# Kernel tuning notes

Measured on AMD Instinct MI355X. Metric: run time of the kernel, lower is better.

## Reference

```python
import jax, jax.numpy as jnp
import numpy as np

B, M, D = 8, 1024, 1024
H = 16
HD = D // H  # 64
F = 4096

def layer_norm(x, gamma, beta, eps=1e-5):
    mu = jnp.mean(x, axis=-1, keepdims=True)
    var = jnp.var(x, axis=-1, keepdims=True)
    return (x - mu) * jax.lax.rsqrt(var + eps) * gamma + beta

def setup_inputs() -> dict:
    key = jax.random.key(0)
    ks = jax.random.split(key, 16)
    s = 0.02
    return {
        "h": jax.random.normal(ks[0], (B, M, D), jnp.float32),
        "h_all": jax.random.normal(ks[1], (B, M, D), jnp.float32),
        "Wq": jax.random.normal(ks[2], (D, D), jnp.float32) * s,
        "Wk": jax.random.normal(ks[3], (D, D), jnp.float32) * s,
        "Wv": jax.random.normal(ks[4], (D, D), jnp.float32) * s,
        "Wo": jax.random.normal(ks[5], (D, D), jnp.float32) * s,
        "W1": jax.random.normal(ks[6], (D, F), jnp.float32) * s,
        "b1": jnp.zeros((F,), jnp.float32),
        "W2": jax.random.normal(ks[7], (F, D), jnp.float32) * s,
        "b2": jnp.zeros((D,), jnp.float32),
        "g1": jnp.ones((D,), jnp.float32),
        "be1": jnp.zeros((D,), jnp.float32),
        "g2": jnp.ones((D,), jnp.float32),
        "be2": jnp.zeros((D,), jnp.float32),
    }

def reference(h, h_all, Wq, Wk, Wv, Wo, W1, b1, W2, b2, g1, be1, g2, be2):
    Bx, Mx, Dx = h.shape
    # projections (no bias, per nn.Linear(bias=False))
    q = (h @ Wq).reshape(Bx, Mx, H, HD)        # [B,M,H,hd]
    k = (h_all @ Wk).reshape(Bx, -1, H, HD)    # [B,N,H,hd]
    v = (h_all @ Wv).reshape(Bx, -1, H, HD)
    # attention: scale by sqrt(head_dim) as in SeqAttention(hidden_size=head_dim)
    scores = jnp.einsum('bqhd,bkhd->bhqk', q, k) / jnp.sqrt(jnp.float32(HD))
    attn = jax.nn.softmax(scores, axis=-1)
    ctx = jnp.einsum('bhqk,bkhd->bqhd', attn, v).reshape(Bx, Mx, Dx)
    attn_out = ctx @ Wo
    # post-norm residual 1
    h1 = layer_norm(h + attn_out, g1, be1)
    # FFN
    ff = jax.nn.relu(h1 @ W1 + b1) @ W2 + b2
    # post-norm residual 2
    out = layer_norm(h1 + ff, g2, be2)
    return out
```

## Files before the change

kernel.cpp:

```cpp
#include <hip/hip_runtime.h>
#include <hip/hip_bf16.h>

#define ROWS 8192
#define DD   1024
#define HH   16
#define HD   64
#define FF   4096

typedef __attribute__((ext_vector_type(4))) float f32x4;
typedef __attribute__((ext_vector_type(8))) __bf16 bf16x8;

static __device__ __forceinline__ unsigned short f2bf(float f) {
  unsigned u = __float_as_uint(f);
  u += 0x7fffu + ((u >> 16) & 1u);
  return (unsigned short)(u >> 16);
}

static __device__ __forceinline__ unsigned cvtpk_bf16(float lo, float hi) {
  unsigned r;
  asm("v_cvt_pk_bf16_f32 %0, %1, %2" : "=v"(r) : "v"(lo), "v"(hi));
  return r;
}

static __device__ __forceinline__ f32x4 mfma16(bf16x8 a, bf16x8 b, f32x4 c) {
  return __builtin_amdgcn_mfma_f32_16x16x32_bf16(a, b, c, 0, 0, 0);
}

#define GLOAD16(gp, lp) __builtin_amdgcn_global_load_lds( \
    (__attribute__((address_space(1))) void*)(gp), \
    (__attribute__((address_space(3))) void*)(lp), 16, 0, 0)

__global__ __launch_bounds__(256) void cast_bf16_k(
    const float* __restrict__ in, unsigned short* __restrict__ out, int n4) {
  int i = blockIdx.x * 256 + threadIdx.x;
  if (i >= n4) return;
  float4 v = ((const float4*)in)[i];
  ushort4 o;
  o.x = f2bf(v.x); o.y = f2bf(v.y); o.z = f2bf(v.z); o.w = f2bf(v.w);
  ((ushort4*)out)[i] = o;
}

__global__ __launch_bounds__(256) void transpose_cast_k(
    const float* __restrict__ in, unsigned short* __restrict__ out, int R, int C) {
  __shared__ float tile[32][33];
  int bx = blockIdx.x * 32;
  int by = blockIdx.y * 32;
  int tx = threadIdx.x, ty = threadIdx.y;
  #pragma unroll
  for (int i = 0; i < 32; i += 8)
    tile[ty + i][tx] = in[(size_t)(by + ty + i) * C + bx + tx];
  __syncthreads();
  #pragma unroll
  for (int i = 0; i < 32; i += 8)
    out[(size_t)(bx + ty + i) * R + by + tx] = f2bf(tile[tx][ty + i]);
}

template <int BM, int MODE, int KS = 1>
__global__ __launch_bounds__(512, 2) void gemm256(
    const unsigned short* __restrict__ A, const unsigned short* __restrict__ BT,
    const float* __restrict__ bias, void* __restrict__ Cout, void* __restrict__ Cout2,
    int Ni, int Ki, int nbx) {
  constexpr int MR = BM / 32;

  const int tid  = threadIdx.x;
  const int lane = tid & 63;
  const int wid  = tid >> 6;
  const int wm   = wid >> 2;
  const int wn   = wid & 3;
  const int lr   = lane & 15;
  const int kq   = lane >> 4;

  const int nwg = gridDim.x;
  const int cpx = nwg >> 3;
  const int wg  = (int)blockIdx.x;
  const int swz = (wg & 7) * cpx + (wg >> 3);
  const int perk = nwg / KS;
  const int kh   = swz / perk;
  const int swzr = swz % perk;
  const int bx = swzr % nbx, by = swzr / nbx;
  const int brow = by * BM, bcol = bx * 256;
  const int Kc   = Ki / KS;
  const int kbase = kh * Kc;

  f32x4 acc[MR][4] = {};
  const int NT = Kc >> 6;

  if constexpr (BM == 256) {
    __shared__ unsigned short As[2 * 2 * 256 * 32];
    __shared__ unsigned short Bs[2 * 2 * 256 * 32];

    const int srow0 = tid >> 2;
    const int csw   = ((tid & 3) ^ ((tid >> 3) & 3)) * 8;
    const size_t sA0 = (size_t)(brow + srow0) * Ki + kbase + csw;
    const size_t sB0 = (size_t)(bcol + srow0) * Ki + kbase + csw;
    const int coff = ((kq ^ ((lr >> 1) & 3)) << 4);

    auto stageu = [&](int srcT, int db, int ks) {
      const size_t so = (size_t)srcT * 64 + ks * 32;
      char* la = (char*)As + (db * 2 + ks) * 16384 + wid * 1024;
      char* lb = (char*)Bs + (db * 2 + ks) * 16384 + wid * 1024;
      GLOAD16(A + sA0 + so, la);
      GLOAD16(A + sA0 + so + (size_t)128 * Ki, la + 8192);
      GLOAD16(BT + sB0 + so, lb);
      GLOAD16(BT + sB0 + so + (size_t)128 * Ki, lb + 8192);
    };

    stageu(0, 0, 0);
    stageu(0, 0, 1);
    stageu(1, 1, 0);

    #pragma unroll 1
    for (int t = 0; t < NT; ++t) {
      const int d = t & 1;
      #pragma unroll
      for (int p = 0; p < 2; ++p) {
        asm volatile("s_waitcnt vmcnt(8)" ::: "memory");
        __builtin_amdgcn_s_barrier();
        __builtin_amdgcn_sched_barrier(0);
        const char* ab = (const char*)As + (d * 2 + p) * 16384;
        const char* bb = (const char*)Bs + (d * 2 + p) * 16384;
        bf16x8 af[8], bfv[4];
        #pragma unroll
        for (int m = 0; m < 8; ++m)
          af[m] = *(const bf16x8*)(ab + (wm * 128 + m * 16 + lr) * 64 + coff);
        #pragma unroll
        for (int n = 0; n < 4; ++n)
          bfv[n] = *(const bf16x8*)(bb + (wn * 64 + n * 16 + lr) * 64 + coff);
        if (p == 0) {
          const int ts = (t + 1 < NT) ? t + 1 : NT - 1;
          stageu(ts, (t + 1) & 1, 1);
        } else {
          const int ts = (t + 2 < NT) ? t + 2 : NT - 1;
          stageu(ts, d, 0);
        }
        __builtin_amdgcn_s_setprio(1);
        #pragma unroll
        for (int m = 0; m < 8; ++m)
          #pragma unroll
          for (int n = 0; n < 4; ++n)
            acc[m][n] = mfma16(af[m], bfv[n], acc[m][n]);
        __builtin_amdgcn_s_setprio(0);
      }
    }
    asm volatile("s_waitcnt vmcnt(0)" ::: "memory");
  } else {
    __shared__ unsigned short As[2][BM * 64];
    __shared__ unsigned short Bs[2][256 * 64];
    const int axor = (lr & 7) << 4;
    const int srow = wid * 8 + (lane >> 3);
    const int scol = ((lane & 7) * 8) ^ ((srow & 7) << 3);
    size_t offA[BM / 64], offB[4];
    #pragma unroll
    for (int L = 0; L < BM / 64; ++L)
      offA[L] = (size_t)(brow + L * 64 + srow) * Ki + kbase + scol;
    #pragma unroll
    for (int L = 0; L < 4; ++L)
      offB[L] = (size_t)(bcol + L * 64 + srow) * Ki + kbase + scol;

    auto stage = [&](int t, int d) {
      #pragma unroll
      for (int L = 0; L < BM / 64; ++L)
        GLOAD16(A + offA[L] + t * 64, (char*)As[d] + L * 8192 + wid * 1024);
      #pragma unroll
      for (int L = 0; L < 4; ++L)
        GLOAD16(BT + offB[L] + t * 64, (char*)Bs[d] + L * 8192 + wid * 1024);
    };

    stage(0, 0);
    stage(1, 1);

    #pragma unroll 1
    for (int t = 0; t < NT; ++t) {
      const int d = t & 1;
      asm volatile("s_waitcnt vmcnt(6)" ::: "memory");
      __builtin_amdgcn_s_barrier();
      __builtin_amdgcn_sched_barrier(0);

      const unsigned short* as = As[d];
      const unsigned short* bs = Bs[d];
      #pragma unroll
      for (int kk = 0; kk < 2; ++kk) {
        bf16x8 af[MR], bfv[4];
        #pragma unroll
        for (int m = 0; m < MR; ++m)
          af[m] = *(const bf16x8*)((const char*)as +
              (wm * (BM / 2) + m * 16 + lr) * 128 + ((kk * 64 + kq * 16) ^ axor));
        #pragma unroll
        for (int n = 0; n < 4; ++n)
          bfv[n] = *(const bf16x8*)((const char*)bs +
              (wn * 64 + n * 16 + lr) * 128 + ((kk * 64 + kq * 16) ^ axor));
        #pragma unroll
        for (int m = 0; m < MR; ++m)
          #pragma unroll
          for (int n = 0; n < 4; ++n)
            acc[m][n] = mfma16(af[m], bfv[n], acc[m][n]);
      }

      asm volatile("s_waitcnt lgkmcnt(0)" ::: "memory");
      __builtin_amdgcn_s_barrier();
      __builtin_amdgcn_sched_barrier(0);
      const int ts = (t + 2 < NT) ? t + 2 : NT - 1;
      stage(ts, d);
    }
  }

  #pragma unroll
  for (int m = 0; m < MR; ++m) {
    #pragma unroll
    for (int n = 0; n < 4; ++n) {
      const int r0 = brow + wm * (BM / 2) + m * 16 + kq * 4;
      const int c  = bcol + wn * 64 + n * 16 + lr;
      if constexpr (MODE == 4) {
        if (c < 1024) {
          #pragma unroll
          for (int e = 0; e < 4; ++e)
            ((unsigned short*)Cout)[(size_t)(r0 + e) * 1024 + c] = f2bf(acc[m][n][e]);
        } else {
          const int cc = c - 1024;
          const int bq = r0 >> 10;
          const int tok = r0 & 1023;
          ushort4 pk;
          pk.x = f2bf(acc[m][n][0]); pk.y = f2bf(acc[m][n][1]);
          pk.z = f2bf(acc[m][n][2]); pk.w = f2bf(acc[m][n][3]);
          *(ushort4*)((unsigned short*)Cout2 + ((size_t)bq * 1024 + cc) * 1024 + tok) = pk;
        }
      } else if constexpr (MODE == 5) {
        float* o = (kh == 0) ? (float*)Cout : (float*)Cout2;
        const float bv = (kh == 0) ? bias[c] : 0.0f;
        #pragma unroll
        for (int e = 0; e < 4; ++e)
          o[(size_t)(r0 + e) * Ni + c] = acc[m][n][e] + bv;
      } else {
        const float bv = (MODE == 2 || MODE == 3) ? bias[c] : 0.0f;
        #pragma unroll
        for (int e = 0; e < 4; ++e) {
          float v = acc[m][n][e] + bv;
          if (MODE == 2) v = fmaxf(v, 0.0f);
          if (MODE == 0 || MODE == 2)
            ((unsigned short*)Cout)[(size_t)(r0 + e) * Ni + c] = f2bf(v);
          else
            ((float*)Cout)[(size_t)(r0 + e) * Ni + c] = v;
        }
      }
    }
  }
}

__global__ __launch_bounds__(512, 6) void attn_k(
    const unsigned short* __restrict__ q, const unsigned short* __restrict__ k,
    const unsigned short* __restrict__ vT, unsigned short* __restrict__ ctx) {
  __shared__ unsigned short Ks[2][64 * 64];
  __shared__ unsigned short Vt[2][64 * 64];
  __shared__ unsigned short Ps[8][16 * 64];
  const int tid = threadIdx.x;
  const int lane = tid & 63;
  const int wid = tid >> 6;
  const int bh = blockIdx.x;
  const int b = bh >> 4, h = bh & 15;
  const int qrow0 = blockIdx.y * 128 + wid * 16;
  const size_t tokbase = (size_t)b * 1024;
  const int lr = lane & 15, kq = lane >> 4;

  const int srow = tid >> 3;
  const int scol = ((tid & 7) * 8) ^ ((srow & 7) << 3);
  const unsigned short* kg = k + (tokbase + srow) * 1024 + h * 64 + scol;
  const unsigned short* vg = vT + ((size_t)(b * 16 + h) * 64 + srow) * 1024 + scol;
  const int ldst = tid * 16;

  auto stage = [&](int kt, int d) {
    GLOAD16(kg + (size_t)kt * 64 * 1024, (char*)Ks[d] + ldst);
    GLOAD16(vg + kt * 64, (char*)Vt[d] + ldst);
  };

  bf16x8 aq[2];
  {
    const unsigned short* qp = q + (tokbase + qrow0 + lr) * DD + h * 64 + kq * 8;
    aq[0] = *(const bf16x8*)qp;
    aq[1] = *(const bf16x8*)(qp + 32);
  }

  float l_acc = 0.f;
  f32x4 acc[4] = {};
  const float C = 0.125f * 1.4426950408889634f;
  const unsigned swp = (unsigned)((lr & 7) << 4);
  const unsigned pbase = (unsigned)(lr * 128);

  stage(0, 0);
  stage(1, 1);

  #pragma unroll 2
  for (int kt = 0; kt < 16; ++kt) {
    const int d = kt & 1;
    asm volatile("s_waitcnt vmcnt(2)" ::: "memory");
    __builtin_amdgcn_s_barrier();
    __builtin_amdgcn_sched_barrier(0);

    f32x4 sv[4] = {};
    #pragma unroll
    for (int jb = 0; jb < 4; ++jb)
      #pragma unroll
      for (int ks = 0; ks < 2; ++ks) {
        int row = jb * 16 + lr;
        bf16x8 ak = *(const bf16x8*)((const char*)Ks[d] +
            row * 128 + ((ks * 64 + kq * 16) ^ ((row & 7) << 4)));
        sv[jb] = mfma16(ak, aq[ks], sv[jb]);
      }

    #pragma unroll
    for (int jb = 0; jb < 4; ++jb) {
      float p0 = exp2f(sv[jb][0] * C);
      float p1 = exp2f(sv[jb][1] * C);
      float p2 = exp2f(sv[jb][2] * C);
      float p3 = exp2f(sv[jb][3] * C);
      l_acc += (p0 + p1) + (p2 + p3);
      uint2 w;
      w.x = cvtpk_bf16(p0, p1);
      w.y = cvtpk_bf16(p2, p3);
      unsigned off = pbase + (((unsigned)(jb * 32 + kq * 8)) ^ swp);
      *(uint2*)((char*)Ps[wid] + off) = w;
    }

    #pragma unroll
    for (int ks = 0; ks < 2; ++ks) {
      bf16x8 ap = *(const bf16x8*)((const char*)Ps[wid] +
          lr * 128 + ((ks * 64 + kq * 16) ^ ((lr & 7) << 4)));
      #pragma unroll
      for (int db = 0; db < 4; ++db) {
        int dd = db * 16 + lr;
        bf16x8 bv = *(const bf16x8*)((const char*)Vt[d] +
            dd * 128 + ((ks * 64 + kq * 16) ^ ((dd & 7) << 4)));
        acc[db] = mfma16(bv, ap, acc[db]);
      }
    }

    asm volatile("s_waitcnt lgkmcnt(0)" ::: "memory");
    __builtin_amdgcn_s_barrier();
    __builtin_amdgcn_sched_barrier(0);
    const int ts = (kt + 2 < 16) ? kt + 2 : 15;
    stage(ts, d);
  }

  float l = l_acc + __shfl_xor(l_acc, 16);
  l += __shfl_xor(l, 32);
  const float inv = 1.0f / l;
  unsigned short* cp = ctx + (tokbase + qrow0 + lr) * DD + h * 64 + kq * 4;
  #pragma unroll
  for (int db = 0; db < 4; ++db) {
    ushort4 o;
    o.x = f2bf(acc[db][0] * inv);
    o.y = f2bf(acc[db][1] * inv);
    o.z = f2bf(acc[db][2] * inv);
    o.w = f2bf(acc[db][3] * inv);
    *(ushort4*)(cp + db * 16) = o;
  }
}

template <int WB>
__global__ __launch_bounds__(256) void ln_add_k(
    const float* __restrict__ a, const float* __restrict__ b,
    const float* __restrict__ gamma, const float* __restrict__ beta,
    float* __restrict__ outf, unsigned short* __restrict__ outb) {
  int row = blockIdx.x;
  int tid = threadIdx.x;
  size_t base = (size_t)row * 1024 + tid * 4;
  float4 va = *(const float4*)(a + base);
  float4 vb = *(const float4*)(b + base);
  float x[4] = {va.x + vb.x, va.y + vb.y, va.z + vb.z, va.w + vb.w};
  float s = x[0] + x[1] + x[2] + x[3];
  float sq = x[0] * x[0] + x[1] * x[1] + x[2] * x[2] + x[3] * x[3];
  #pragma unroll
  for (int mk = 1; mk < 64; mk <<= 1) {
    s += __shfl_xor(s, mk);
    sq += __shfl_xor(sq, mk);
  }
  __shared__ float red[8];
  int wid = tid >> 6, lane = tid & 63;
  if (lane == 0) { red[wid] = s; red[4 + wid] = sq; }
  __syncthreads();
  s = red[0] + red[1] + red[2] + red[3];
  sq = red[4] + red[5] + red[6] + red[7];
  float mu = s * (1.0f / 1024.0f);
  float var = sq * (1.0f / 1024.0f) - mu * mu;
  float rs = rsqrtf(var + 1e-5f);
  float4 g = *(const float4*)(gamma + tid * 4);
  float4 be = *(const float4*)(beta + tid * 4);
  float y[4];
  y[0] = (x[0] - mu) * rs * g.x + be.x;
  y[1] = (x[1] - mu) * rs * g.y + be.y;
  y[2] = (x[2] - mu) * rs * g.z + be.z;
  y[3] = (x[3] - mu) * rs * g.w + be.w;
  float4 o; o.x = y[0]; o.y = y[1]; o.z = y[2]; o.w = y[3];
  *(float4*)(outf + base) = o;
  if (WB) {
    ushort4 ob;
    ob.x = f2bf(y[0]); ob.y = f2bf(y[1]); ob.z = f2bf(y[2]); ob.w = f2bf(y[3]);
    *(ushort4*)(outb + base) = ob;
  }
}

__global__ __launch_bounds__(256) void ln3_k(
    const float* __restrict__ a, const float* __restrict__ b,
    const float* __restrict__ c,
    const float* __restrict__ gamma, const float* __restrict__ beta,
    float* __restrict__ outf) {
  int row = blockIdx.x;
  int tid = threadIdx.x;
  size_t base = (size_t)row * 1024 + tid * 4;
  float4 va = *(const float4*)(a + base);
  float4 vb = *(const float4*)(b + base);
  float4 vc = *(const float4*)(c + base);
  float x[4] = {va.x + vb.x + vc.x, va.y + vb.y + vc.y,
                va.z + vb.z + vc.z, va.w + vb.w + vc.w};
  float s = x[0] + x[1] + x[2] + x[3];
  float sq = x[0] * x[0] + x[1] * x[1] + x[2] * x[2] + x[3] * x[3];
  #pragma unroll
  for (int mk = 1; mk < 64; mk <<= 1) {
    s += __shfl_xor(s, mk);
    sq += __shfl_xor(sq, mk);
  }
  __shared__ float red[8];
  int wid = tid >> 6, lane = tid & 63;
  if (lane == 0) { red[wid] = s; red[4 + wid] = sq; }
  __syncthreads();
  s = red[0] + red[1] + red[2] + red[3];
  sq = red[4] + red[5] + red[6] + red[7];
  float mu = s * (1.0f / 1024.0f);
  float var = sq * (1.0f / 1024.0f) - mu * mu;
  float rs = rsqrtf(var + 1e-5f);
  float4 g = *(const float4*)(gamma + tid * 4);
  float4 be = *(const float4*)(beta + tid * 4);
  float4 o;
  o.x = (x[0] - mu) * rs * g.x + be.x;
  o.y = (x[1] - mu) * rs * g.y + be.y;
  o.z = (x[2] - mu) * rs * g.z + be.z;
  o.w = (x[3] - mu) * rs * g.w + be.w;
  *(float4*)(outf + base) = o;
}

extern "C" void kernel_launch(void* const* d_in, const int* in_sizes, int n_in,
                              void* d_out, int out_size, void* d_ws, size_t ws_size,
                              hipStream_t stream) {
  const float* h    = (const float*)d_in[0];
  const float* hall = (const float*)d_in[1];
  const float* Wq   = (const float*)d_in[2];
  const float* Wk   = (const float*)d_in[3];
  const float* Wv   = (const float*)d_in[4];
  const float* Wo   = (const float*)d_in[5];
  const float* W1   = (const float*)d_in[6];
  const float* b1   = (const float*)d_in[7];
  const float* W2   = (const float*)d_in[8];
  const float* b2   = (const float*)d_in[9];
  const float* g1   = (const float*)d_in[10];
  const float* be1  = (const float*)d_in[11];
  const float* g2   = (const float*)d_in[12];
  const float* be2  = (const float*)d_in[13];

  char* ws = (char*)d_ws;
  size_t off = 0;
  auto alloc = [&](size_t n) { size_t o = off; off += (n + 255) & ~(size_t)255; return o; };
  const size_t hb_o   = alloc((size_t)ROWS * DD * 2);
  const size_t hab_o  = alloc((size_t)ROWS * DD * 2);
  const size_t wqt_o  = alloc((size_t)DD * DD * 2);
  const size_t wkvt_o = alloc((size_t)DD * DD * 4);
  const size_t wot_o  = alloc((size_t)DD * DD * 2);
  const size_t w1t_o  = alloc((size_t)DD * FF * 2);
  const size_t w2t_o  = alloc((size_t)FF * DD * 2);
  const size_t qb_o   = alloc((size_t)ROWS * DD * 2);
  const size_t kb_o   = alloc((size_t)ROWS * DD * 2);
  const size_t vt_o   = alloc((size_t)ROWS * DD * 2);
  const size_t cx_o   = alloc((size_t)ROWS * DD * 2);
  const size_t h1_o   = alloc((size_t)ROWS * DD * 4);
  const size_t h1b_o  = alloc((size_t)ROWS * DD * 2);

  unsigned short* hb   = (unsigned short*)(ws + hb_o);
  unsigned short* hab  = (unsigned short*)(ws + hab_o);
  unsigned short* wqt  = (unsigned short*)(ws + wqt_o);
  unsigned short* wkvt = (unsigned short*)(ws + wkvt_o);
  unsigned short* wot  = (unsigned short*)(ws + wot_o);
  unsigned short* w1t  = (unsigned short*)(ws + w1t_o);
  unsigned short* w2t  = (unsigned short*)(ws + w2t_o);
  unsigned short* qb   = (unsigned short*)(ws + qb_o);
  unsigned short* kb   = (unsigned short*)(ws + kb_o);
  unsigned short* vTb  = (unsigned short*)(ws + vt_o);
  unsigned short* cxb  = (unsigned short*)(ws + cx_o);
  float*          h1   = (float*)(ws + h1_o);
  unsigned short* h1b  = (unsigned short*)(ws + h1b_o);
  float*          attn_out = (float*)(ws + hb_o);
  float*          ff2p1    = (float*)(ws + hb_o);
  unsigned short* ff1      = (unsigned short*)(ws + qb_o);
  float*          outf     = (float*)d_out;

  cast_bf16_k<<<ROWS * DD / 1024, 256, 0, stream>>>(h, hb, ROWS * DD / 4);
  cast_bf16_k<<<ROWS * DD / 1024, 256, 0, stream>>>(hall, hab, ROWS * DD / 4);
  dim3 tb(32, 8);
  transpose_cast_k<<<dim3(32, 32), tb, 0, stream>>>(Wq, wqt, DD, DD);
  transpose_cast_k<<<dim3(32, 32), tb, 0, stream>>>(Wk, wkvt, DD, DD);
  transpose_cast_k<<<dim3(32, 32), tb, 0, stream>>>(Wv, wkvt + (size_t)DD * DD, DD, DD);
  transpose_cast_k<<<dim3(32, 32), tb, 0, stream>>>(Wo, wot, DD, DD);
  transpose_cast_k<<<dim3(128, 32), tb, 0, stream>>>(W1, w1t, DD, FF);
  transpose_cast_k<<<dim3(32, 128), tb, 0, stream>>>(W2, w2t, FF, DD);

  gemm256<128, 0><<<dim3(256), 512, 0, stream>>>(hb,  wqt,  nullptr, qb, nullptr, DD,   DD, 4);
  gemm256<256, 4><<<dim3(256), 512, 0, stream>>>(hab, wkvt, nullptr, kb, vTb,    2048, DD, 8);

  attn_k<<<dim3(128, 8), 512, 0, stream>>>(qb, kb, vTb, cxb);

  gemm256<128, 1><<<dim3(256), 512, 0, stream>>>(cxb, wot, nullptr, attn_out, nullptr, DD, DD, 4);
  ln_add_k<1><<<ROWS, 256, 0, stream>>>(h, attn_out, g1, be1, h1, h1b);

  gemm256<256, 2>   <<<dim3(512), 512, 0, stream>>>(h1b, w1t, b1, ff1, nullptr, FF, DD, 16);
  gemm256<256, 5, 2><<<dim3(256), 512, 0, stream>>>(ff1, w2t, b2, outf, ff2p1, DD, FF, 4);

  ln3_k<<<ROWS, 256, 0, stream>>>(h1, outf, ff2p1, g2, be2, outf);
}
```

Baseline: 384.7 us.

## Store residual intermediates in bf16 and merge prep casts into one kernel

Merges the eight cast/transpose launches into a single prep kernel that dispatches on block index. The attention output projection, the h1 residual and the split-K partial of the second FFN GEMM are now stored as bf16 rather than fp32. The first LayerNorm reads the bf16 copy of h, and the final LayerNorm reads bf16 h1. This cuts memory traffic and launch overhead, but the residual path loses precision, which may push error close to tolerance.

```diff
diff --git a/kernel.cpp b/kernel.cpp
--- a/kernel.cpp
+++ b/kernel.cpp
@@ -16,6 +16,10 @@
   return (unsigned short)(u >> 16);
 }
 
+static __device__ __forceinline__ float bf2f(unsigned short u) {
+  return __uint_as_float(((unsigned)u) << 16);
+}
+
 static __device__ __forceinline__ unsigned cvtpk_bf16(float lo, float hi) {
   unsigned r;
   asm("v_cvt_pk_bf16_f32 %0, %1, %2" : "=v"(r) : "v"(lo), "v"(hi));
@@ -30,29 +34,56 @@
     (__attribute__((address_space(1))) void*)(gp), \
     (__attribute__((address_space(3))) void*)(lp), 16, 0, 0)
 
-__global__ __launch_bounds__(256) void cast_bf16_k(
-    const float* __restrict__ in, unsigned short* __restrict__ out, int n4) {
-  int i = blockIdx.x * 256 + threadIdx.x;
-  if (i >= n4) return;
-  float4 v = ((const float4*)in)[i];
-  ushort4 o;
-  o.x = f2bf(v.x); o.y = f2bf(v.y); o.z = f2bf(v.z); o.w = f2bf(v.w);
-  ((ushort4*)out)[i] = o;
-}
-
-__global__ __launch_bounds__(256) void transpose_cast_k(
-    const float* __restrict__ in, unsigned short* __restrict__ out, int R, int C) {
+__global__ __launch_bounds__(256) void prep_k(
+    const float* __restrict__ h, const float* __restrict__ hall,
+    const float* __restrict__ Wq, const float* __restrict__ Wk,
+    const float* __restrict__ Wv, const float* __restrict__ Wo,
+    const float* __restrict__ W1, const float* __restrict__ W2,
+    unsigned short* __restrict__ hb, unsigned short* __restrict__ hab,
+    unsigned short* __restrict__ wqt, unsigned short* __restrict__ wkvt,
+    unsigned short* __restrict__ wot, unsigned short* __restrict__ w1t,
+    unsigned short* __restrict__ w2t) {
   __shared__ float tile[32][33];
-  int bx = blockIdx.x * 32;
-  int by = blockIdx.y * 32;
-  int tx = threadIdx.x, ty = threadIdx.y;
+  const int bid = blockIdx.x;
+  const int tid = threadIdx.x;
+
+  if (bid < 16384) {
+    const float* src = (bid < 8192) ? h : hall;
+    unsigned short* dst = (bid < 8192) ? hb : hab;
+    int i = (bid & 8191) * 256 + tid;
+    float4 v = ((const float4*)src)[i];
+    ushort4 o;
+    o.x = f2bf(v.x); o.y = f2bf(v.y); o.z = f2bf(v.z); o.w = f2bf(v.w);
+    ((ushort4*)dst)[i] = o;
+    return;
+  }
+
+  int r = bid - 16384;
+  const float* src; unsigned short* dst; int R, C, bx, by;
+  if (r < 4096) {
+    int which = r >> 10, idx = r & 1023;
+    R = C = 1024; bx = idx & 31; by = idx >> 5;
+    if (which == 0) { src = Wq; dst = wqt; }
+    else if (which == 1) { src = Wk; dst = wkvt; }
+    else if (which == 2) { src = Wv; dst = wkvt + (size_t)DD * DD; }
+    else { src = Wo; dst = wot; }
+  } else if (r < 8192) {
+    int idx = r - 4096;
+    R = 1024; C = 4096; bx = idx & 127; by = idx >> 7;
+    src = W1; dst = w1t;
+  } else {
+    int idx = r - 8192;
+    R = 4096; C = 1024; bx = idx & 31; by = idx >> 5;
+    src = W2; dst = w2t;
+  }
+  const int tx = tid & 31, ty = tid >> 5;
   #pragma unroll
   for (int i = 0; i < 32; i += 8)
-    tile[ty + i][tx] = in[(size_t)(by + ty + i) * C + bx + tx];
+    tile[ty + i][tx] = src[(size_t)(by * 32 + ty + i) * C + bx * 32 + tx];
   __syncthreads();
   #pragma unroll
   for (int i = 0; i < 32; i += 8)
-    out[(size_t)(bx + ty + i) * R + by + tx] = f2bf(tile[tx][ty + i]);
+    dst[(size_t)(bx * 32 + ty + i) * R + by * 32 + tx] = f2bf(tile[tx][ty + i]);
 }
 
 template <int BM, int MODE, int KS = 1>
@@ -225,11 +256,16 @@
           *(ushort4*)((unsigned short*)Cout2 + ((size_t)bq * 1024 + cc) * 1024 + tok) = pk;
         }
       } else if constexpr (MODE == 5) {
-        float* o = (kh == 0) ? (float*)Cout : (float*)Cout2;
-        const float bv = (kh == 0) ? bias[c] : 0.0f;
-        #pragma unroll
-        for (int e = 0; e < 4; ++e)
-          o[(size_t)(r0 + e) * Ni + c] = acc[m][n][e] + bv;
+        if (kh == 0) {
+          const float bv = bias[c];
+          #pragma unroll
+          for (int e = 0; e < 4; ++e)
+            ((float*)Cout)[(size_t)(r0 + e) * Ni + c] = acc[m][n][e] + bv;
+        } else {
+          #pragma unroll
+          for (int e = 0; e < 4; ++e)
+            ((unsigned short*)Cout2)[(size_t)(r0 + e) * Ni + c] = f2bf(acc[m][n][e]);
+        }
       } else {
         const float bv = (MODE == 2 || MODE == 3) ? bias[c] : 0.0f;
         #pragma unroll
@@ -355,17 +391,17 @@
   }
 }
 
-template <int WB>
-__global__ __launch_bounds__(256) void ln_add_k(
-    const float* __restrict__ a, const float* __restrict__ b,
+__global__ __launch_bounds__(256) void ln_add_bb_k(
+    const unsigned short* __restrict__ a, const unsigned short* __restrict__ b,
     const float* __restrict__ gamma, const float* __restrict__ beta,
-    float* __restrict__ outf, unsigned short* __restrict__ outb) {
+    unsigned short* __restrict__ outb) {
   int row = blockIdx.x;
   int tid = threadIdx.x;
   size_t base = (size_t)row * 1024 + tid * 4;
-  float4 va = *(const float4*)(a + base);
-  float4 vb = *(const float4*)(b + base);
-  float x[4] = {va.x + vb.x, va.y + vb.y, va.z + vb.z, va.w + vb.w};
+  ushort4 va = *(const ushort4*)(a + base);
+  ushort4 vb = *(const ushort4*)(b + base);
+  float x[4] = {bf2f(va.x) + bf2f(vb.x), bf2f(va.y) + bf2f(vb.y),
+                bf2f(va.z) + bf2f(vb.z), bf2f(va.w) + bf2f(vb.w)};
   float s = x[0] + x[1] + x[2] + x[3];
   float sq = x[0] * x[0] + x[1] * x[1] + x[2] * x[2] + x[3] * x[3];
   #pragma unroll
@@ -384,33 +420,27 @@
   float rs = rsqrtf(var + 1e-5f);
   float4 g = *(const float4*)(gamma + tid * 4);
   float4 be = *(const float4*)(beta + tid * 4);
-  float y[4];
-  y[0] = (x[0] - mu) * rs * g.x + be.x;
-  y[1] = (x[1] - mu) * rs * g.y + be.y;
-  y[2] = (x[2] - mu) * rs * g.z + be.z;
-  y[3] = (x[3] - mu) * rs * g.w + be.w;
-  float4 o; o.x = y[0]; o.y = y[1]; o.z = y[2]; o.w = y[3];
-  *(float4*)(outf + base) = o;
-  if (WB) {
-    ushort4 ob;
-    ob.x = f2bf(y[0]); ob.y = f2bf(y[1]); ob.z = f2bf(y[2]); ob.w = f2bf(y[3]);
-    *(ushort4*)(outb + base) = ob;
-  }
+  ushort4 ob;
+  ob.x = f2bf((x[0] - mu) * rs * g.x + be.x);
+  ob.y = f2bf((x[1] - mu) * rs * g.y + be.y);
+  ob.z = f2bf((x[2] - mu) * rs * g.z + be.z);
+  ob.w = f2bf((x[3] - mu) * rs * g.w + be.w);
+  *(ushort4*)(outb + base) = ob;
 }
 
 __global__ __launch_bounds__(256) void ln3_k(
-    const float* __restrict__ a, const float* __restrict__ b,
-    const float* __restrict__ c,
+    const unsigned short* __restrict__ a, const float* __restrict__ b,
+    const unsigned short* __restrict__ c,
     const float* __restrict__ gamma, const float* __restrict__ beta,
     float* __restrict__ outf) {
   int row = blockIdx.x;
   int tid = threadIdx.x;
   size_t base = (size_t)row * 1024 + tid * 4;
-  float4 va = *(const float4*)(a + base);
+  ushort4 va = *(const ushort4*)(a + base);
   float4 vb = *(const float4*)(b + base);
-  float4 vc = *(const float4*)(c + base);
-  float x[4] = {va.x + vb.x + vc.x, va.y + vb.y + vc.y,
-                va.z + vb.z + vc.z, va.w + vb.w + vc.w};
+  ushort4 vc = *(const ushort4*)(c + base);
+  float x[4] = {bf2f(va.x) + vb.x + bf2f(vc.x), bf2f(va.y) + vb.y + bf2f(vc.y),
+                bf2f(va.z) + vb.z + bf2f(vc.z), bf2f(va.w) + vb.w + bf2f(vc.w)};
   float s = x[0] + x[1] + x[2] + x[3];
   float sq = x[0] * x[0] + x[1] * x[1] + x[2] * x[2] + x[3] * x[3];
   #pragma unroll
@@ -469,8 +499,8 @@
   const size_t kb_o   = alloc((size_t)ROWS * DD * 2);
   const size_t vt_o   = alloc((size_t)ROWS * DD * 2);
   const size_t cx_o   = alloc((size_t)ROWS * DD * 2);
-  const size_t h1_o   = alloc((size_t)ROWS * DD * 4);
   const size_t h1b_o  = alloc((size_t)ROWS * DD * 2);
+  const size_t fp1_o  = alloc((size_t)ROWS * DD * 2);
 
   unsigned short* hb   = (unsigned short*)(ws + hb_o);
   unsigned short* hab  = (unsigned short*)(ws + hab_o);
@@ -483,33 +513,25 @@
   unsigned short* kb   = (unsigned short*)(ws + kb_o);
   unsigned short* vTb  = (unsigned short*)(ws + vt_o);
   unsigned short* cxb  = (unsigned short*)(ws + cx_o);
-  float*          h1   = (float*)(ws + h1_o);
   unsigned short* h1b  = (unsigned short*)(ws + h1b_o);
-  float*          attn_out = (float*)(ws + hb_o);
-  float*          ff2p1    = (float*)(ws + hb_o);
-  unsigned short* ff1      = (unsigned short*)(ws + qb_o);
-  float*          outf     = (float*)d_out;
-
-  cast_bf16_k<<<ROWS * DD / 1024, 256, 0, stream>>>(h, hb, ROWS * DD / 4);
-  cast_bf16_k<<<ROWS * DD / 1024, 256, 0, stream>>>(hall, hab, ROWS * DD / 4);
-  dim3 tb(32, 8);
-  transpose_cast_k<<<dim3(32, 32), tb, 0, stream>>>(Wq, wqt, DD, DD);
-  transpose_cast_k<<<dim3(32, 32), tb, 0, stream>>>(Wk, wkvt, DD, DD);
-  transpose_cast_k<<<dim3(32, 32), tb, 0, stream>>>(Wv, wkvt + (size_t)DD * DD, DD, DD);
-  transpose_cast_k<<<dim3(32, 32), tb, 0, stream>>>(Wo, wot, DD, DD);
-  transpose_cast_k<<<dim3(128, 32), tb, 0, stream>>>(W1, w1t, DD, FF);
-  transpose_cast_k<<<dim3(32, 128), tb, 0, stream>>>(W2, w2t, FF, DD);
+  unsigned short* fp1b = (unsigned short*)(ws + fp1_o);
+  unsigned short* attn_ob = (unsigned short*)(ws + hab_o);
+  unsigned short* ff1     = (unsigned short*)(ws + qb_o);
+  float*          outf    = (float*)d_out;
+
+  prep_k<<<dim3(16384 + 4096 + 4096 + 4096), 256, 0, stream>>>(
+      h, hall, Wq, Wk, Wv, Wo, W1, W2, hb, hab, wqt, wkvt, wot, w1t, w2t);
 
   gemm256<128, 0><<<dim3(256), 512, 0, stream>>>(hb,  wqt,  nullptr, qb, nullptr, DD,   DD, 4);
   gemm256<256, 4><<<dim3(256), 512, 0, stream>>>(hab, wkvt, nullptr, kb, vTb,    2048, DD, 8);
 
   attn_k<<<dim3(128, 8), 512, 0, stream>>>(qb, kb, vTb, cxb);
 
-  gemm256<128, 1><<<dim3(256), 512, 0, stream>>>(cxb, wot, nullptr, attn_out, nullptr, DD, DD, 4);
-  ln_add_k<1><<<ROWS, 256, 0, stream>>>(h, attn_out, g1, be1, h1, h1b);
+  gemm256<128, 0><<<dim3(256), 512, 0, stream>>>(cxb, wot, nullptr, attn_ob, nullptr, DD, DD, 4);
+  ln_add_bb_k<<<ROWS, 256, 0, stream>>>(hb, attn_ob, g1, be1, h1b);
 
   gemm256<256, 2>   <<<dim3(512), 512, 0, stream>>>(h1b, w1t, b1, ff1, nullptr, FF, DD, 16);
-  gemm256<256, 5, 2><<<dim3(256), 512, 0, stream>>>(ff1, w2t, b2, outf, ff2p1, DD, FF, 4);
-
-  ln3_k<<<ROWS, 256, 0, stream>>>(h1, outf, ff2p1, g2, be2, outf);
-}
+  gemm256<256, 5, 2><<<dim3(256), 512, 0, stream>>>(ff1, w2t, b2, outf, fp1b, DD, FF, 4);
+
+  ln3_k<<<ROWS, 256, 0, stream>>>(h1b, outf, fp1b, g2, be2, outf);
+}
```

Result: faster. 360.0 us (-6.4%).
